# Optimization experiments

Measured on AMD Instinct MI355X. Metric: run time of the kernel, lower is better.

## Reference

```python
import jax, jax.numpy as jnp
import numpy as np

NEG = -1e30  # log(0) surrogate, safe for fp32 logaddexp
BLANK = 0


def setup_inputs() -> dict:
    key = jax.random.key(0)
    k1, k2, k3 = jax.random.split(key, 3)
    T, B, C, S = 1024, 128, 256, 64
    logits = jax.random.normal(k1, (T, B, C), dtype=jnp.float32)
    log_probs = jax.nn.log_softmax(logits, axis=-1)  # CTCLoss expects log-probs
    targets = jax.random.randint(k2, (B, S), 1, C)          # labels in [1, C-1], blank excluded
    target_lengths = jax.random.randint(k3, (B,), 1, S + 1)  # lengths in [1, S]
    return {"log_probs": log_probs, "targets": targets, "target_lengths": target_lengths}


def _ctc_loss(log_probs, targets, target_lengths):
    """CTC loss, blank=0, reduction='mean' (per-sample loss / target_len, then batch mean),
    zero_infinity=True, input_lengths = T for every batch element (as in the wrapper)."""
    T, B, C = log_probs.shape
    S = targets.shape[1]
    L = 2 * S + 1  # extended label length (blanks interleaved)

    # Extended label sequence: [blank, t0, blank, t1, ..., t_{S-1}, blank]  -> (B, L)
    ext = jnp.full((B, L), BLANK, dtype=targets.dtype)
    ext = ext.at[:, 1::2].set(targets)

    # Skip transition (s-2 -> s) allowed iff ext[s] != blank and ext[s] != ext[s-2]
    ext_m2 = jnp.concatenate([jnp.full((B, 2), BLANK, dtype=ext.dtype), ext[:, :-2]], axis=1)
    skip = (ext != BLANK) & (ext != ext_m2)
    skip = skip.at[:, :2].set(False)

    # alpha init at t=0
    lp0 = jnp.take_along_axis(log_probs[0], ext, axis=1)  # (B, L)
    alpha0 = jnp.full((B, L), NEG, dtype=log_probs.dtype)
    alpha0 = alpha0.at[:, 0].set(lp0[:, 0]).at[:, 1].set(lp0[:, 1])

    neg_col = jnp.full((B, 1), NEG, dtype=log_probs.dtype)

    def step(alpha, lp_t):
        lp_ext = jnp.take_along_axis(lp_t, ext, axis=1)            # (B, L)
        p1 = jnp.concatenate([neg_col, alpha[:, :-1]], axis=1)     # alpha[s-1]
        p2 = jnp.concatenate([neg_col, neg_col, alpha[:, :-2]], axis=1)  # alpha[s-2]
        a = jnp.logaddexp(alpha, p1)
        a = jnp.where(skip, jnp.logaddexp(a, p2), a)
        return a + lp_ext, None

    alpha, _ = jax.lax.scan(step, alpha0, log_probs[1:])  # (B, L)

    # Terminal states: s = 2*len and s = 2*len - 1
    idx_last = (2 * target_lengths)[:, None]
    a_last = jnp.take_along_axis(alpha, idx_last, axis=1)[:, 0]
    a_prev = jnp.take_along_axis(alpha, idx_last - 1, axis=1)[:, 0]
    loss = -jnp.logaddexp(a_last, a_prev)  # (B,)

    # zero_infinity=True: infinite (or NEG-saturated) losses -> 0
    loss = jnp.where(jnp.isfinite(loss) & (loss < 1e29), loss, 0.0)

    # reduction='mean': divide each loss by its target length, then mean over batch
    return jnp.mean(loss / target_lengths.astype(loss.dtype))


def reference(log_probs, targets, target_lengths):
    return _ctc_loss(log_probs, targets, target_lengths)
```

## Files before the change

kernel.cpp:

```cpp
#include <hip/hip_runtime.h>
#include <math.h>

#define LOG2E  1.4426950408889634f
#define LN2    0.6931471805599453f

#define T_DIM 1024
#define B_DIM 128
#define C_DIM 256
#define S_DIM 64
#define CH 16
#define NCHD 32
#define RBN 3
#define PBN 3

__device__ __forceinline__ float fexp2(float x) { return __builtin_amdgcn_exp2f(x); }
__device__ __forceinline__ float flog2(float x) { return __builtin_amdgcn_logf(x); }

__device__ __forceinline__ int dpp_shr1_i(int x) {
    return __builtin_amdgcn_update_dpp(0, x, 0x138, 0xF, 0xF, false);
}
__device__ __forceinline__ int dpp_shl1_i(int x) {
    return __builtin_amdgcn_update_dpp(0, x, 0x130, 0xF, 0xF, false);
}
template <int C> __device__ __forceinline__ float dpp_maxf(float m) {
    int s = __builtin_amdgcn_update_dpp(__float_as_int(m), __float_as_int(m),
                                        C, 0xF, 0xF, false);
    return fmaxf(m, __int_as_float(s));
}
template <int C> __device__ __forceinline__ float dpp_addf(float v) {
    int s = __builtin_amdgcn_update_dpp(0, __float_as_int(v), C, 0xF, 0xF, false);
    return v + __int_as_float(s);
}

#define GLOAD_LDS16(gp, lp)                                                    \
    __builtin_amdgcn_global_load_lds(                                          \
        (const __attribute__((address_space(1))) void*)(gp),                   \
        (__attribute__((address_space(3))) void*)(lp), 16, 0, 0)

#define VMWAIT(N_) asm volatile("s_waitcnt vmcnt(" #N_ ")" ::: "memory")
#define LGKM0()    asm volatile("s_waitcnt lgkmcnt(0)" ::: "memory")
#define FENCE()                                                                \
    do { __builtin_amdgcn_sched_barrier(0);                                    \
         asm volatile("" ::: "memory"); } while (0)

__global__ __launch_bounds__(512) void ctc_alpha_kernel(
    const float* __restrict__ log_probs,
    const int* __restrict__ targets,
    const int* __restrict__ target_lengths,
    float* __restrict__ per_batch)
{
    const int b = blockIdx.x;
    const int tid = threadIdx.x;
    const int lane = tid & 63;
    const int wid = tid >> 6;

    __shared__ float  rbF[RBN][CH][C_DIM];
    __shared__ float  rbB[RBN][CH][C_DIM];
    __shared__ float2 pcF[PBN][CH][64];
    __shared__ float2 pcB[PBN][CH][64];
    __shared__ float gam0[64], gam1[64];
    __shared__ int   gelB[64];
    __shared__ float gam2s;
    __shared__ int sfF, cvEF, cvOF, cfF, sfB, cvEB, cvOB, cfB;

    const int e1 = targets[b * S_DIM + lane];
    const int ep = (lane > 0) ? targets[b * S_DIM + lane - 1] : 0;
    const bool skipf = (lane > 0) && (e1 != ep);
    const int en = dpp_shl1_i(e1);
    const bool skipb = (lane < 63) && (en != e1);
    const bool is63 = (lane == 63);
    const int len = target_lengths[b];

    const float* base = log_probs + (size_t)b * C_DIM;
    const size_t stride = (size_t)B_DIM * C_DIM;

    if (tid == 0) {
        sfF = 0; cvEF = 0; cvOF = 0; cfF = 0;
        sfB = 0; cvEB = 0; cvOB = 0; cfB = 0;
    }
    __syncthreads();

    volatile int* vsfF = &sfF; volatile int* vcEF = &cvEF;
    volatile int* vcOF = &cvOF; volatile int* vcfF = &cfF;
    volatile int* vsfB = &sfB; volatile int* vcEB = &cvEB;
    volatile int* vcOB = &cvOB; volatile int* vcfB = &cfB;

#define STAGER_BODY(RB_, VSF_, VCE_, VCO_, T0_, SGN_)                          \
    do {                                                                       \
        for (int c = 0; c < NCHD; ++c) {                                       \
            if (c >= RBN) {                                                    \
                const int d_ = c - RBN;                                        \
                if (d_ & 1) { while (*VCO_ < (d_ + 1) / 2) __builtin_amdgcn_s_sleep(1); } \
                else        { while (*VCE_ < d_ / 2 + 1) __builtin_amdgcn_s_sleep(1); }  \
                FENCE();                                                       \
            }                                                                  \
            const int rb_ = c % RBN;                                           \
            _Pragma("unroll")                                                  \
            for (int k_ = 0; k_ < CH; ++k_) {                                  \
                const int t_ = (T0_) + (SGN_) * (16 * c + k_);                 \
                GLOAD_LDS16(base + (size_t)t_ * stride + 4 * lane,             \
                            &RB_[rb_][k_][0]);                                 \
            }                                                                  \
            VMWAIT(32);                                                        \
            FENCE();                                                           \
            if (c >= 2 && lane == 0) *VSF_ = c - 1;                            \
        }                                                                      \
        VMWAIT(16); FENCE(); if (lane == 0) *VSF_ = NCHD - 1;                  \
        VMWAIT(0);  FENCE(); if (lane == 0) *VSF_ = NCHD;                      \
    } while (0)

#define CONV_BODY(RB_, PC_, VSF_, VMYF_, VCF_, PAR_)                           \
    do {                                                                       \
        for (int c = PAR_; c < NCHD; c += 2) {                                 \
            while (*VSF_ < c + 1) { }                                          \
            if (c >= PBN) {                                                    \
                while (*VCF_ < c - PBN + 1) __builtin_amdgcn_s_sleep(1);       \
            }                                                                  \
            FENCE();                                                           \
            const int rb_ = c % RBN;                                           \
            const int pb_ = c % PBN;                                           \
            _Pragma("unroll")                                                  \
            for (int k_ = 0; k_ < CH; ++k_) {                                  \
                float pl_ = RB_[rb_][k_][e1];                                  \
                float pbl_ = RB_[rb_][k_][0];                                  \
                float2 v_;                                                     \
                v_.x = fexp2(pl_ * LOG2E);                                     \
                v_.y = fexp2(pbl_ * LOG2E);                                    \
                PC_[pb_][k_][lane] = v_;                                       \
            }                                                                  \
            LGKM0();                                                           \
            if (lane == 0) *VMYF_ = (PAR_) ? (c + 1) / 2 : c / 2 + 1;          \
        }                                                                      \
    } while (0)

#define POLLG(VCE_, VCO_, C_)                                                  \
    do { const int cc_ = (C_);                                                 \
         if (cc_ & 1) { while (*VCO_ < (cc_ + 1) / 2) { } }                    \
         else         { while (*VCE_ < cc_ / 2 + 1) { } }                      \
         FENCE(); } while (0)

#define GATHER_G(PC_, PLX, PBX, SLOT)                                          \
    do { _Pragma("unroll")                                                     \
         for (int k_ = 0; k_ < CH; ++k_) {                                     \
             float2 v_ = PC_[SLOT][k_][lane];                                  \
             PLX[k_] = v_.x; PBX[k_] = v_.y;                                   \
         } } while (0)

    if (wid == 1) {
        STAGER_BODY(rbF, vsfF, vcEF, vcOF, 1, 1);
    } else if (wid == 5) {
        STAGER_BODY(rbB, vsfB, vcEB, vcOB, 1022, -1);
    } else if (wid == 2) {
        CONV_BODY(rbF, pcF, vsfF, vcEF, vcfF, 0);
    } else if (wid == 3) {
        CONV_BODY(rbF, pcF, vsfF, vcOF, vcfF, 1);
    } else if (wid == 6) {
        CONV_BODY(rbB, pcB, vsfB, vcEB, vcfB, 0);
    } else if (wid == 7) {
        CONV_BODY(rbB, pcB, vsfB, vcOB, vcfB, 1);
    } else if (wid == 0) {
        float a0, a1, a2; int el = 0, dexp = 0;
        {
            float i0 = base[0], ie = base[e1];
            a0 = (lane == 0) ? fexp2(i0 * LOG2E) : 0.0f;
            a1 = (lane == 0) ? fexp2(ie * LOG2E) : 0.0f;
            a2 = 0.0f;
        }
#define RESCALE_F()                                                            \
    do { float mx_ = fmaxf(a0, fmaxf(a1, a2));                                 \
         int eb_ = (int)((__float_as_uint(mx_) >> 23) & 0xFFu) - 127;          \
         el += eb_;                                                            \
         float sc_ = __uint_as_float((unsigned)(127 - eb_) << 23);             \
         a0 *= sc_; a1 *= sc_; a2 *= sc_; } while (0)
#define ACT_STEP_F(PBV, PLV, K_)                                               \
    do { float am1_ = __int_as_float(dpp_shr1_i(__float_as_int(a1)));          \
         int eprev_ = dpp_shr1_i(el);                                          \
         int iz_ = __float_as_int(a0) | __float_as_int(a1) |                   \
                   __float_as_int(a2);                                         \
         int ele_ = (iz_ == 0) ? eprev_ : el;                                  \
         float am1s_ = ldexpf(am1_, eprev_ - ele_);                            \
         el = ele_;                                                            \
         float n0_ = (a0 + am1s_) * (PBV);                                     \
         float s2_ = skipf ? am1s_ : 0.0f;                                     \
         float n1_ = (a1 + a0 + s2_) * (PLV);                                  \
         float n2_ = (a2 + a1) * (PBV);                                        \
         a0 = n0_; a1 = n1_; a2 = n2_;                                         \
         if (((K_) & 3) == 3) RESCALE_F(); } while (0)
#define STREAM_STEP_F(PBV, PLV)                                                \
    do { float am1_ = __int_as_float(dpp_shr1_i(__float_as_int(a1)));          \
         float am1s_ = ldexpf(am1_, dexp);                                     \
         float n0_ = (a0 + am1s_) * (PBV);                                     \
         float s2_ = skipf ? am1s_ : 0.0f;                                     \
         float n1_ = (a1 + a0 + s2_) * (PLV);                                  \
         float n2_ = (a2 + a1) * (PBV);                                        \
         a0 = n0_; a1 = n1_; a2 = n2_; } while (0)
#define ACT_FROM_F(PLX, PBX)                                                   \
    do { _Pragma("unroll")                                                     \
         for (int k_ = 0; k_ < CH; ++k_) ACT_STEP_F(PBX[k_], PLX[k_], k_);     \
    } while (0)
#define STREAM_FROM_F(PLX, PBX)                                                \
    do { _Pragma("unroll")                                                     \
         for (int q_ = 0; q_ < 4; ++q_) {                                      \
             dexp = dpp_shr1_i(el) - el;                                       \
             STREAM_STEP_F(PBX[4 * q_ + 0], PLX[4 * q_ + 0]);                  \
             STREAM_STEP_F(PBX[4 * q_ + 1], PLX[4 * q_ + 1]);                  \
             STREAM_STEP_F(PBX[4 * q_ + 2], PLX[4 * q_ + 2]);                  \
             STREAM_STEP_F(PBX[4 * q_ + 3], PLX[4 * q_ + 3]);                  \
             RESCALE_F(); } } while (0)
#define TAIL_FROM_F(PLX, PBX)                                                  \
    do { _Pragma("unroll")                                                     \
         for (int q_ = 0; q_ < 3; ++q_) {                                      \
             dexp = dpp_shr1_i(el) - el;                                       \
             STREAM_STEP_F(PBX[4 * q_ + 0], PLX[4 * q_ + 0]);                  \
             STREAM_STEP_F(PBX[4 * q_ + 1], PLX[4 * q_ + 1]);                  \
             STREAM_STEP_F(PBX[4 * q_ + 2], PLX[4 * q_ + 2]);                  \
             STREAM_STEP_F(PBX[4 * q_ + 3], PLX[4 * q_ + 3]);                  \
             RESCALE_F(); }                                                    \
         dexp = dpp_shr1_i(el) - el;                                           \
         STREAM_STEP_F(PBX[12], PLX[12]);                                      \
         STREAM_STEP_F(PBX[13], PLX[13]);                                      \
         STREAM_STEP_F(PBX[14], PLX[14]); } while (0)

        float plA[CH], pbA[CH], plB[CH], pbB[CH];
        POLLG(vcEF, vcOF, 0);
        GATHER_G(pcF, plA, pbA, 0);
        for (int c = 0; c < 10; c += 2) {
            POLLG(vcEF, vcOF, c + 1);
            GATHER_G(pcF, plB, pbB, (c + 1) % PBN);
            ACT_FROM_F(plA, pbA);
            if (lane == 0) *vcfF = c + 1;
            POLLG(vcEF, vcOF, c + 2);
            GATHER_G(pcF, plA, pbA, (c + 2) % PBN);
            ACT_FROM_F(plB, pbB);
            if (lane == 0) *vcfF = c + 2;
        }
        for (int c = 10; c < 30; c += 2) {
            POLLG(vcEF, vcOF, c + 1);
            GATHER_G(pcF, plB, pbB, (c + 1) % PBN);
            STREAM_FROM_F(plA, pbA);
            if (lane == 0) *vcfF = c + 1;
            POLLG(vcEF, vcOF, c + 2);
            GATHER_G(pcF, plA, pbA, (c + 2) % PBN);
            STREAM_FROM_F(plB, pbB);
            if (lane == 0) *vcfF = c + 2;
        }
        POLLG(vcEF, vcOF, NCHD - 1);
        GATHER_G(pcF, plB, pbB, (NCHD - 1) % PBN);
        STREAM_FROM_F(plA, pbA);
        if (lane == 0) *vcfF = NCHD - 1;
        TAIL_FROM_F(plB, pbB);
        if (lane == 0) *vcfF = NCHD;

        __syncthreads();

        float la0 = flog2(a0) + (float)el;
        float la1 = flog2(a1) + (float)el;
        float g0 = gam0[lane], g1 = gam1[lane];
        float eB = (float)gelB[lane];
        float q0 = la0 + flog2(g0) + eB;
        float q1 = la1 + flog2(g1) + eB;
        float q2 = is63 ? (flog2(a2) + (float)el + flog2(gam2s) + eB) : -1e30f;
        q0 = fmaxf(q0, -1e30f); q1 = fmaxf(q1, -1e30f); q2 = fmaxf(q2, -1e30f);
        float ml = fmaxf(q0, fmaxf(q1, q2));
        float lw = ml + flog2(fexp2(q0 - ml) + fexp2(q1 - ml) + fexp2(q2 - ml));
        float m_ = lw;
        m_ = dpp_maxf<0x111>(m_); m_ = dpp_maxf<0x112>(m_);
        m_ = dpp_maxf<0x114>(m_); m_ = dpp_maxf<0x118>(m_);
        m_ = dpp_maxf<0x142>(m_); m_ = dpp_maxf<0x143>(m_);
        float M = __int_as_float(__builtin_amdgcn_readlane(__float_as_int(m_), 63));
        float v_ = fexp2(lw - M);
        v_ = dpp_addf<0x111>(v_); v_ = dpp_addf<0x112>(v_);
        v_ = dpp_addf<0x114>(v_); v_ = dpp_addf<0x118>(v_);
        v_ = dpp_addf<0x142>(v_); v_ = dpp_addf<0x143>(v_);
        float S = __int_as_float(__builtin_amdgcn_readlane(__float_as_int(v_), 63));
        if (lane == 0) {
            float lse2 = M + flog2(S);
            float loss = -(lse2 * LN2);
            if (!isfinite(loss) || !(loss < 1e29f)) loss = 0.0f;
            per_batch[b] = loss / (float)len;
        }
    } else {
        float b0, b1, b2; int elB = 0, dexB = 0, dex0 = 0;
        {
            const float* rowT = base + (size_t)(T_DIM - 1) * stride;
            float lpb_ = rowT[0], lpl_ = rowT[e1];
            b1 = (lane == len - 1) ? fexp2(lpl_ * LOG2E) : 0.0f;
            b0 = (lane == len && len < S_DIM) ? fexp2(lpb_ * LOG2E) : 0.0f;
            b2 = (len == S_DIM && is63) ? fexp2(lpb_ * LOG2E) : 0.0f;
        }
#define RESCALE_B()                                                            \
    do { float mx_ = fmaxf(b0, fmaxf(b1, b2));                                 \
         int eb_ = (int)((__float_as_uint(mx_) >> 23) & 0xFFu) - 127;          \
         elB += eb_;                                                           \
         float sc_ = __uint_as_float((unsigned)(127 - eb_) << 23);             \
         b0 *= sc_; b1 *= sc_; b2 *= sc_; } while (0)
#define ACT_STEP_B(PBV, PLV, K_)                                               \
    do { float nb0_ = __int_as_float(dpp_shl1_i(__float_as_int(b0)));          \
         nb0_ = is63 ? b2 : nb0_;                                              \
         float nb1_ = __int_as_float(dpp_shl1_i(__float_as_int(b1)));          \
         int en_ = dpp_shl1_i(elB);                                            \
         int iz_ = __float_as_int(b0) | __float_as_int(b1) |                   \
                   __float_as_int(b2);                                         \
         int eln_ = (iz_ == 0) ? en_ : elB;                                    \
         int d0_ = is63 ? (elB - eln_) : (en_ - eln_);                         \
         float nb0a_ = ldexpf(nb0_, d0_);                                      \
         float nb1a_ = ldexpf(nb1_, en_ - eln_);                               \
         elB = eln_;                                                           \
         float n0_ = (b0 + b1) * (PBV);                                        \
         float n1_ = (b1 + nb0a_ + (skipb ? nb1a_ : 0.0f)) * (PLV);            \
         float n2_ = b2 * (PBV);                                               \
         b0 = n0_; b1 = n1_; b2 = n2_;                                         \
         if (((K_) & 3) == 3) RESCALE_B(); } while (0)
#define STREAM_STEP_B(PBV, PLV)                                                \
    do { float nb0_ = __int_as_float(dpp_shl1_i(__float_as_int(b0)));          \
         nb0_ = is63 ? b2 : nb0_;                                              \
         float nb1_ = __int_as_float(dpp_shl1_i(__float_as_int(b1)));          \
         float nb0a_ = ldexpf(nb0_, dex0);                                     \
         float nb1a_ = ldexpf(nb1_, dexB);                                     \
         float n0_ = (b0 + b1) * (PBV);                                        \
         float n1_ = (b1 + nb0a_ + (skipb ? nb1a_ : 0.0f)) * (PLV);            \
         float n2_ = b2 * (PBV);                                               \
         b0 = n0_; b1 = n1_; b2 = n2_; } while (0)
#define SET_DEX_B()                                                            \
    do { dexB = dpp_shl1_i(elB) - elB; dex0 = is63 ? 0 : dexB; } while (0)
#define ACT_FROM_B(PLX, PBX)                                                   \
    do { _Pragma("unroll")                                                     \
         for (int k_ = 0; k_ < CH; ++k_) ACT_STEP_B(PBX[k_], PLX[k_], k_);     \
    } while (0)
#define STREAM_FROM_B(PLX, PBX)                                                \
    do { _Pragma("unroll")                                                     \
         for (int q_ = 0; q_ < 4; ++q_) {                                      \
             SET_DEX_B();                                                      \
             STREAM_STEP_B(PBX[4 * q_ + 0], PLX[4 * q_ + 0]);                  \
             STREAM_STEP_B(PBX[4 * q_ + 1], PLX[4 * q_ + 1]);                  \
             STREAM_STEP_B(PBX[4 * q_ + 2], PLX[4 * q_ + 2]);                  \
             STREAM_STEP_B(PBX[4 * q_ + 3], PLX[4 * q_ + 3]);                  \
             RESCALE_B(); } } while (0)
#define TAIL_FROM_B(PLX, PBX)                                                  \
    do { _Pragma("unroll")                                                     \
         for (int q_ = 0; q_ < 3; ++q_) {                                      \
             SET_DEX_B();                                                      \
             STREAM_STEP_B(PBX[4 * q_ + 0], PLX[4 * q_ + 0]);                  \
             STREAM_STEP_B(PBX[4 * q_ + 1], PLX[4 * q_ + 1]);                  \
             STREAM_STEP_B(PBX[4 * q_ + 2], PLX[4 * q_ + 2]);                  \
             STREAM_STEP_B(PBX[4 * q_ + 3], PLX[4 * q_ + 3]);                  \
             RESCALE_B(); }                                                    \
         SET_DEX_B();                                                          \
         STREAM_STEP_B(PBX[12], PLX[12]);                                      \
         STREAM_STEP_B(PBX[13], PLX[13]);                                      \
         STREAM_STEP_B(PBX[14], PLX[14]); } while (0)

        float plA[CH], pbA[CH], plB[CH], pbB[CH];
        POLLG(vcEB, vcOB, 0);
        GATHER_G(pcB, plA, pbA, 0);
        for (int c = 0; c < 10; c += 2) {
            POLLG(vcEB, vcOB, c + 1);
            GATHER_G(pcB, plB, pbB, (c + 1) % PBN);
            ACT_FROM_B(plA, pbA);
            if (lane == 0) *vcfB = c + 1;
            POLLG(vcEB, vcOB, c + 2);
            GATHER_G(pcB, plA, pbA, (c + 2) % PBN);
            ACT_FROM_B(plB, pbB);
            if (lane == 0) *vcfB = c + 2;
        }
        for (int c = 10; c < 30; c += 2) {
            POLLG(vcEB, vcOB, c + 1);
            GATHER_G(pcB, plB, pbB, (c + 1) % PBN);
            STREAM_FROM_B(plA, pbA);
            if (lane == 0) *vcfB = c + 1;
            POLLG(vcEB, vcOB, c + 2);
            GATHER_G(pcB, plA, pbA, (c + 2) % PBN);
            STREAM_FROM_B(plB, pbB);
            if (lane == 0) *vcfB = c + 2;
        }
        POLLG(vcEB, vcOB, NCHD - 1);
        GATHER_G(pcB, plB, pbB, (NCHD - 1) % PBN);
        STREAM_FROM_B(plA, pbA);
        if (lane == 0) *vcfB = NCHD - 1;
        TAIL_FROM_B(plB, pbB);
        if (lane == 0) *vcfB = NCHD;

        {
            float nb0_ = __int_as_float(dpp_shl1_i(__float_as_int(b0)));
            nb0_ = is63 ? b2 : nb0_;
            float nb1_ = __int_as_float(dpp_shl1_i(__float_as_int(b1)));
            int en_ = dpp_shl1_i(elB);
            int d_ = is63 ? 0 : (en_ - elB);
            float nb0a_ = ldexpf(nb0_, d_);
            float nb1a_ = ldexpf(nb1_, d_);
            gam0[lane] = b0 + b1;
            gam1[lane] = b1 + nb0a_ + (skipb ? nb1a_ : 0.0f);
            gelB[lane] = elB;
            if (is63) gam2s = b2;
        }
        __syncthreads();
    }

    if (wid != 0 && wid != 4) __syncthreads();
}

__global__ __launch_bounds__(64) void ctc_reduce_kernel(
    const float* __restrict__ per_batch, float* __restrict__ out)
{
    const int lane = threadIdx.x;
    float v = per_batch[lane] + per_batch[lane + 64];
    #pragma unroll
    for (int off = 32; off > 0; off >>= 1) {
        v += __shfl_down(v, off, 64);
    }
    if (lane == 0) out[0] = v / (float)B_DIM;
}

extern "C" void kernel_launch(void* const* d_in, const int* in_sizes, int n_in,
                              void* d_out, int out_size, void* d_ws, size_t ws_size,
                              hipStream_t stream) {
    const float* log_probs = (const float*)d_in[0];
    const int* targets = (const int*)d_in[1];
    const int* target_lengths = (const int*)d_in[2];
    float* out = (float*)d_out;
    float* per_batch = (float*)d_ws;

    ctc_alpha_kernel<<<B_DIM, 512, 0, stream>>>(log_probs, targets,
                                                target_lengths, per_batch);
    ctc_reduce_kernel<<<1, 64, 0, stream>>>(per_batch, out);
}
```

Baseline: 45.38 us.

## Split forward and backward CTC scans into separate workgroups, combine in second kernel

The single 512-thread block that ran both the forward alpha and backward beta recursions for one batch element is split into two 256-thread blocks, one per direction, giving 256 workgroups instead of 128. Each block writes log-domain boundary values to workspace, and a new combine kernel does the per-sample logsumexp, zero_infinity handling and batch mean, replacing the in-block meet and reduce. LDS ring depths are raised (RBN 4, PBN 6) because each block now holds only one direction's buffers. This aims to spread the serial scans across more CUs, at the cost of a global-memory round trip and a heavier final kernel that serially loops over 16 samples per wave.

```diff
diff --git a/kernel.cpp b/kernel.cpp
--- a/kernel.cpp
+++ b/kernel.cpp
@@ -10,8 +10,8 @@
 #define S_DIM 64
 #define CH 16
 #define NCHD 32
-#define RBN 3
-#define PBN 3
+#define RBN 4
+#define PBN 6
 
 __device__ __forceinline__ float fexp2(float x) { return __builtin_amdgcn_exp2f(x); }
 __device__ __forceinline__ float flog2(float x) { return __builtin_amdgcn_logf(x); }
@@ -21,15 +21,6 @@
 }
 __device__ __forceinline__ int dpp_shl1_i(int x) {
     return __builtin_amdgcn_update_dpp(0, x, 0x130, 0xF, 0xF, false);
-}
-template <int C> __device__ __forceinline__ float dpp_maxf(float m) {
-    int s = __builtin_amdgcn_update_dpp(__float_as_int(m), __float_as_int(m),
-                                        C, 0xF, 0xF, false);
-    return fmaxf(m, __int_as_float(s));
-}
-template <int C> __device__ __forceinline__ float dpp_addf(float v) {
-    int s = __builtin_amdgcn_update_dpp(0, __float_as_int(v), C, 0xF, 0xF, false);
-    return v + __int_as_float(s);
 }
 
 #define GLOAD_LDS16(gp, lp)                                                    \
@@ -43,25 +34,22 @@
     do { __builtin_amdgcn_sched_barrier(0);                                    \
          asm volatile("" ::: "memory"); } while (0)
 
-__global__ __launch_bounds__(512) void ctc_alpha_kernel(
+__global__ __launch_bounds__(256) void ctc_scan_kernel(
     const float* __restrict__ log_probs,
     const int* __restrict__ targets,
     const int* __restrict__ target_lengths,
-    float* __restrict__ per_batch)
+    float* __restrict__ ws)
 {
-    const int b = blockIdx.x;
+    const int bx = blockIdx.x;
+    const int b = bx >> 1;
+    const int dir = bx & 1;
     const int tid = threadIdx.x;
     const int lane = tid & 63;
     const int wid = tid >> 6;
 
-    __shared__ float  rbF[RBN][CH][C_DIM];
-    __shared__ float  rbB[RBN][CH][C_DIM];
-    __shared__ float2 pcF[PBN][CH][64];
-    __shared__ float2 pcB[PBN][CH][64];
-    __shared__ float gam0[64], gam1[64];
-    __shared__ int   gelB[64];
-    __shared__ float gam2s;
-    __shared__ int sfF, cvEF, cvOF, cfF, sfB, cvEB, cvOB, cfB;
+    __shared__ float  rbuf[RBN][CH][C_DIM];
+    __shared__ float2 pcv[PBN][CH][64];
+    __shared__ int sf, cvE, cvO, cf;
 
     const int e1 = targets[b * S_DIM + lane];
     const int ep = (lane > 0) ? targets[b * S_DIM + lane - 1] : 0;
@@ -74,91 +62,72 @@
     const float* base = log_probs + (size_t)b * C_DIM;
     const size_t stride = (size_t)B_DIM * C_DIM;
 
-    if (tid == 0) {
-        sfF = 0; cvEF = 0; cvOF = 0; cfF = 0;
-        sfB = 0; cvEB = 0; cvOB = 0; cfB = 0;
-    }
+    if (tid == 0) { sf = 0; cvE = 0; cvO = 0; cf = 0; }
     __syncthreads();
 
-    volatile int* vsfF = &sfF; volatile int* vcEF = &cvEF;
-    volatile int* vcOF = &cvOF; volatile int* vcfF = &cfF;
-    volatile int* vsfB = &sfB; volatile int* vcEB = &cvEB;
-    volatile int* vcOB = &cvOB; volatile int* vcfB = &cfB;
-
-#define STAGER_BODY(RB_, VSF_, VCE_, VCO_, T0_, SGN_)                          \
-    do {                                                                       \
-        for (int c = 0; c < NCHD; ++c) {                                       \
-            if (c >= RBN) {                                                    \
-                const int d_ = c - RBN;                                        \
-                if (d_ & 1) { while (*VCO_ < (d_ + 1) / 2) __builtin_amdgcn_s_sleep(1); } \
-                else        { while (*VCE_ < d_ / 2 + 1) __builtin_amdgcn_s_sleep(1); }  \
-                FENCE();                                                       \
-            }                                                                  \
-            const int rb_ = c % RBN;                                           \
-            _Pragma("unroll")                                                  \
-            for (int k_ = 0; k_ < CH; ++k_) {                                  \
-                const int t_ = (T0_) + (SGN_) * (16 * c + k_);                 \
-                GLOAD_LDS16(base + (size_t)t_ * stride + 4 * lane,             \
-                            &RB_[rb_][k_][0]);                                 \
-            }                                                                  \
-            VMWAIT(32);                                                        \
-            FENCE();                                                           \
-            if (c >= 2 && lane == 0) *VSF_ = c - 1;                            \
-        }                                                                      \
-        VMWAIT(16); FENCE(); if (lane == 0) *VSF_ = NCHD - 1;                  \
-        VMWAIT(0);  FENCE(); if (lane == 0) *VSF_ = NCHD;                      \
-    } while (0)
-
-#define CONV_BODY(RB_, PC_, VSF_, VMYF_, VCF_, PAR_)                           \
-    do {                                                                       \
-        for (int c = PAR_; c < NCHD; c += 2) {                                 \
-            while (*VSF_ < c + 1) { }                                          \
-            if (c >= PBN) {                                                    \
-                while (*VCF_ < c - PBN + 1) __builtin_amdgcn_s_sleep(1);       \
-            }                                                                  \
-            FENCE();                                                           \
-            const int rb_ = c % RBN;                                           \
-            const int pb_ = c % PBN;                                           \
-            _Pragma("unroll")                                                  \
-            for (int k_ = 0; k_ < CH; ++k_) {                                  \
-                float pl_ = RB_[rb_][k_][e1];                                  \
-                float pbl_ = RB_[rb_][k_][0];                                  \
-                float2 v_;                                                     \
-                v_.x = fexp2(pl_ * LOG2E);                                     \
-                v_.y = fexp2(pbl_ * LOG2E);                                    \
-                PC_[pb_][k_][lane] = v_;                                       \
-            }                                                                  \
-            LGKM0();                                                           \
-            if (lane == 0) *VMYF_ = (PAR_) ? (c + 1) / 2 : c / 2 + 1;          \
-        }                                                                      \
-    } while (0)
-
-#define POLLG(VCE_, VCO_, C_)                                                  \
+    volatile int* vsf = &sf; volatile int* vcE = &cvE;
+    volatile int* vcO = &cvO; volatile int* vcf = &cf;
+
+    const int t0d = dir ? 1022 : 1;
+    const int sgn = dir ? -1 : 1;
+
+#define POLLG(C_)                                                              \
     do { const int cc_ = (C_);                                                 \
-         if (cc_ & 1) { while (*VCO_ < (cc_ + 1) / 2) { } }                    \
-         else         { while (*VCE_ < cc_ / 2 + 1) { } }                      \
+         if (cc_ & 1) { while (*vcO < (cc_ + 1) / 2) { } }                     \
+         else         { while (*vcE < cc_ / 2 + 1) { } }                       \
          FENCE(); } while (0)
 
-#define GATHER_G(PC_, PLX, PBX, SLOT)                                          \
+#define GATHER_G(PLX, PBX, SLOT)                                               \
     do { _Pragma("unroll")                                                     \
          for (int k_ = 0; k_ < CH; ++k_) {                                     \
-             float2 v_ = PC_[SLOT][k_][lane];                                  \
+             float2 v_ = pcv[SLOT][k_][lane];                                  \
              PLX[k_] = v_.x; PBX[k_] = v_.y;                                   \
          } } while (0)
 
     if (wid == 1) {
-        STAGER_BODY(rbF, vsfF, vcEF, vcOF, 1, 1);
-    } else if (wid == 5) {
-        STAGER_BODY(rbB, vsfB, vcEB, vcOB, 1022, -1);
-    } else if (wid == 2) {
-        CONV_BODY(rbF, pcF, vsfF, vcEF, vcfF, 0);
-    } else if (wid == 3) {
-        CONV_BODY(rbF, pcF, vsfF, vcOF, vcfF, 1);
-    } else if (wid == 6) {
-        CONV_BODY(rbB, pcB, vsfB, vcEB, vcfB, 0);
-    } else if (wid == 7) {
-        CONV_BODY(rbB, pcB, vsfB, vcOB, vcfB, 1);
-    } else if (wid == 0) {
+        for (int c = 0; c < NCHD; ++c) {
+            if (c >= RBN) {
+                const int d_ = c - RBN;
+                if (d_ & 1) { while (*vcO < (d_ + 1) / 2) __builtin_amdgcn_s_sleep(1); }
+                else        { while (*vcE < d_ / 2 + 1) __builtin_amdgcn_s_sleep(1); }
+                FENCE();
+            }
+            const int rb_ = c & (RBN - 1);
+            #pragma unroll
+            for (int k_ = 0; k_ < CH; ++k_) {
+                const int t_ = t0d + sgn * (16 * c + k_);
+                GLOAD_LDS16(base + (size_t)t_ * stride + 4 * lane,
+                            &rbuf[rb_][k_][0]);
+            }
+            VMWAIT(32);
+            FENCE();
+            if (c >= 2 && lane == 0) *vsf = c - 1;
+        }
+        VMWAIT(16); FENCE(); if (lane == 0) *vsf = NCHD - 1;
+        VMWAIT(0);  FENCE(); if (lane == 0) *vsf = NCHD;
+    } else if (wid >= 2) {
+        const int par = wid - 2;
+        for (int c = par; c < NCHD; c += 2) {
+            while (*vsf < c + 1) { }
+            if (c >= PBN) {
+                while (*vcf < c - PBN + 1) __builtin_amdgcn_s_sleep(1);
+            }
+            FENCE();
+            const int rb_ = c & (RBN - 1);
+            const int pb_ = c % PBN;
+            #pragma unroll
+            for (int k_ = 0; k_ < CH; ++k_) {
+                float pl_ = rbuf[rb_][k_][e1];
+                float pbl_ = rbuf[rb_][k_][0];
+                float2 v_;
+                v_.x = fexp2(pl_ * LOG2E);
+                v_.y = fexp2(pbl_ * LOG2E);
+                pcv[pb_][k_][lane] = v_;
+            }
+            LGKM0();
+            if (lane == 0) { if (par) *vcO = (c + 1) / 2; else *vcE = c / 2 + 1; }
+        }
+    } else if (dir == 0) {
         float a0, a1, a2; int el = 0, dexp = 0;
         {
             float i0 = base[0], ie = base[e1];
@@ -222,63 +191,31 @@
          STREAM_STEP_F(PBX[14], PLX[14]); } while (0)
 
         float plA[CH], pbA[CH], plB[CH], pbB[CH];
-        POLLG(vcEF, vcOF, 0);
-        GATHER_G(pcF, plA, pbA, 0);
+        POLLG(0);
+        GATHER_G(plA, pbA, 0);
         for (int c = 0; c < 10; c += 2) {
-            POLLG(vcEF, vcOF, c + 1);
-            GATHER_G(pcF, plB, pbB, (c + 1) % PBN);
-            ACT_FROM_F(plA, pbA);
-            if (lane == 0) *vcfF = c + 1;
-            POLLG(vcEF, vcOF, c + 2);
-            GATHER_G(pcF, plA, pbA, (c + 2) % PBN);
-            ACT_FROM_F(plB, pbB);
-            if (lane == 0) *vcfF = c + 2;
+            POLLG(c + 1); GATHER_G(plB, pbB, (c + 1) % PBN);
+            ACT_FROM_F(plA, pbA); if (lane == 0) *vcf = c + 1;
+            POLLG(c + 2); GATHER_G(plA, pbA, (c + 2) % PBN);
+            ACT_FROM_F(plB, pbB); if (lane == 0) *vcf = c + 2;
         }
         for (int c = 10; c < 30; c += 2) {
-            POLLG(vcEF, vcOF, c + 1);
-            GATHER_G(pcF, plB, pbB, (c + 1) % PBN);
-            STREAM_FROM_F(plA, pbA);
-            if (lane == 0) *vcfF = c + 1;
-            POLLG(vcEF, vcOF, c + 2);
-            GATHER_G(pcF, plA, pbA, (c + 2) % PBN);
-            STREAM_FROM_F(plB, pbB);
-            if (lane == 0) *vcfF = c + 2;
-        }
-        POLLG(vcEF, vcOF, NCHD - 1);
-        GATHER_G(pcF, plB, pbB, (NCHD - 1) % PBN);
+            POLLG(c + 1); GATHER_G(plB, pbB, (c + 1) % PBN);
+            STREAM_FROM_F(plA, pbA); if (lane == 0) *vcf = c + 1;
+            POLLG(c + 2); GATHER_G(plA, pbA, (c + 2) % PBN);
+            STREAM_FROM_F(plB, pbB); if (lane == 0) *vcf = c + 2;
+        }
+        POLLG(NCHD - 1);
+        GATHER_G(plB, pbB, (NCHD - 1) % PBN);
         STREAM_FROM_F(plA, pbA);
-        if (lane == 0) *vcfF = NCHD - 1;
+        if (lane == 0) *vcf = NCHD - 1;
         TAIL_FROM_F(plB, pbB);
-        if (lane == 0) *vcfF = NCHD;
-
-        __syncthreads();
-
-        float la0 = flog2(a0) + (float)el;
-        float la1 = flog2(a1) + (float)el;
-        float g0 = gam0[lane], g1 = gam1[lane];
-        float eB = (float)gelB[lane];
-        float q0 = la0 + flog2(g0) + eB;
-        float q1 = la1 + flog2(g1) + eB;
-        float q2 = is63 ? (flog2(a2) + (float)el + flog2(gam2s) + eB) : -1e30f;
-        q0 = fmaxf(q0, -1e30f); q1 = fmaxf(q1, -1e30f); q2 = fmaxf(q2, -1e30f);
-        float ml = fmaxf(q0, fmaxf(q1, q2));
-        float lw = ml + flog2(fexp2(q0 - ml) + fexp2(q1 - ml) + fexp2(q2 - ml));
-        float m_ = lw;
-        m_ = dpp_maxf<0x111>(m_); m_ = dpp_maxf<0x112>(m_);
-        m_ = dpp_maxf<0x114>(m_); m_ = dpp_maxf<0x118>(m_);
-        m_ = dpp_maxf<0x142>(m_); m_ = dpp_maxf<0x143>(m_);
-        float M = __int_as_float(__builtin_amdgcn_readlane(__float_as_int(m_), 63));
-        float v_ = fexp2(lw - M);
-        v_ = dpp_addf<0x111>(v_); v_ = dpp_addf<0x112>(v_);
-        v_ = dpp_addf<0x114>(v_); v_ = dpp_addf<0x118>(v_);
-        v_ = dpp_addf<0x142>(v_); v_ = dpp_addf<0x143>(v_);
-        float S = __int_as_float(__builtin_amdgcn_readlane(__float_as_int(v_), 63));
-        if (lane == 0) {
-            float lse2 = M + flog2(S);
-            float loss = -(lse2 * LN2);
-            if (!isfinite(loss) || !(loss < 1e29f)) loss = 0.0f;
-            per_batch[b] = loss / (float)len;
-        }
+        if (lane == 0) *vcf = NCHD;
+
+        float* oF = ws + (size_t)b * 129;
+        oF[lane] = flog2(a0) + (float)el;
+        oF[64 + lane] = flog2(a1) + (float)el;
+        if (is63) oF[128] = flog2(a2) + (float)el;
     } else {
         float b0, b1, b2; int elB = 0, dexB = 0, dex0 = 0;
         {
@@ -351,34 +288,26 @@
          STREAM_STEP_B(PBX[14], PLX[14]); } while (0)
 
         float plA[CH], pbA[CH], plB[CH], pbB[CH];
-        POLLG(vcEB, vcOB, 0);
-        GATHER_G(pcB, plA, pbA, 0);
+        POLLG(0);
+        GATHER_G(plA, pbA, 0);
         for (int c = 0; c < 10; c += 2) {
-            POLLG(vcEB, vcOB, c + 1);
-            GATHER_G(pcB, plB, pbB, (c + 1) % PBN);
-            ACT_FROM_B(plA, pbA);
-            if (lane == 0) *vcfB = c + 1;
-            POLLG(vcEB, vcOB, c + 2);
-            GATHER_G(pcB, plA, pbA, (c + 2) % PBN);
-            ACT_FROM_B(plB, pbB);
-            if (lane == 0) *vcfB = c + 2;
+            POLLG(c + 1); GATHER_G(plB, pbB, (c + 1) % PBN);
+            ACT_FROM_B(plA, pbA); if (lane == 0) *vcf = c + 1;
+            POLLG(c + 2); GATHER_G(plA, pbA, (c + 2) % PBN);
+            ACT_FROM_B(plB, pbB); if (lane == 0) *vcf = c + 2;
         }
         for (int c = 10; c < 30; c += 2) {
-            POLLG(vcEB, vcOB, c + 1);
-            GATHER_G(pcB, plB, pbB, (c + 1) % PBN);
-            STREAM_FROM_B(plA, pbA);
-            if (lane == 0) *vcfB = c + 1;
-            POLLG(vcEB, vcOB, c + 2);
-            GATHER_G(pcB, plA, pbA, (c + 2) % PBN);
-            STREAM_FROM_B(plB, pbB);
-            if (lane == 0) *vcfB = c + 2;
-        }
-        POLLG(vcEB, vcOB, NCHD - 1);
-        GATHER_G(pcB, plB, pbB, (NCHD - 1) % PBN);
+            POLLG(c + 1); GATHER_G(plB, pbB, (c + 1) % PBN);
+            STREAM_FROM_B(plA, pbA); if (lane == 0) *vcf = c + 1;
+            POLLG(c + 2); GATHER_G(plA, pbA, (c + 2) % PBN);
+            STREAM_FROM_B(plB, pbB); if (lane == 0) *vcf = c + 2;
+        }
+        POLLG(NCHD - 1);
+        GATHER_G(plB, pbB, (NCHD - 1) % PBN);
         STREAM_FROM_B(plA, pbA);
-        if (lane == 0) *vcfB = NCHD - 1;
+        if (lane == 0) *vcf = NCHD - 1;
         TAIL_FROM_B(plB, pbB);
-        if (lane == 0) *vcfB = NCHD;
+        if (lane == 0) *vcf = NCHD;
 
         {
             float nb0_ = __int_as_float(dpp_shl1_i(__float_as_int(b0)));
@@ -388,27 +317,57 @@
             int d_ = is63 ? 0 : (en_ - elB);
             float nb0a_ = ldexpf(nb0_, d_);
             float nb1a_ = ldexpf(nb1_, d_);
-            gam0[lane] = b0 + b1;
-            gam1[lane] = b1 + nb0a_ + (skipb ? nb1a_ : 0.0f);
-            gelB[lane] = elB;
-            if (is63) gam2s = b2;
-        }
-        __syncthreads();
+            float g0 = b0 + b1;
+            float g1 = b1 + nb0a_ + (skipb ? nb1a_ : 0.0f);
+            float* oB = ws + (size_t)(B_DIM * 129) + (size_t)b * 129;
+            oB[lane] = flog2(g0) + (float)elB;
+            oB[64 + lane] = flog2(g1) + (float)elB;
+            if (is63) oB[128] = flog2(b2) + (float)elB;
+        }
     }
-
-    if (wid != 0 && wid != 4) __syncthreads();
-}
-
-__global__ __launch_bounds__(64) void ctc_reduce_kernel(
-    const float* __restrict__ per_batch, float* __restrict__ out)
+}
+
+__global__ __launch_bounds__(512) void ctc_combine_kernel(
+    const float* __restrict__ ws,
+    const int* __restrict__ target_lengths,
+    float* __restrict__ out)
 {
-    const int lane = threadIdx.x;
-    float v = per_batch[lane] + per_batch[lane + 64];
-    #pragma unroll
-    for (int off = 32; off > 0; off >>= 1) {
-        v += __shfl_down(v, off, 64);
+    const int tid = threadIdx.x;
+    const int lane = tid & 63;
+    const int w = tid >> 6;
+    __shared__ float part[8];
+
+    float acc = 0.0f;
+    for (int i = 0; i < 16; ++i) {
+        const int b = w * 16 + i;
+        const float* F = ws + (size_t)b * 129;
+        const float* G = ws + (size_t)(B_DIM * 129) + (size_t)b * 129;
+        float q0 = F[lane] + G[lane];
+        float q1 = F[64 + lane] + G[64 + lane];
+        float q2 = (lane == 63) ? (F[128] + G[128]) : -1e30f;
+        float m = fmaxf(q0, fmaxf(q1, q2));
+        #pragma unroll
+        for (int off = 1; off < 64; off <<= 1) {
+            m = fmaxf(m, __shfl_xor(m, off, 64));
+        }
+        float s = fexp2(q0 - m) + fexp2(q1 - m) + fexp2(q2 - m);
+        #pragma unroll
+        for (int off = 1; off < 64; off <<= 1) {
+            s += __shfl_xor(s, off, 64);
+        }
+        float lse2 = m + flog2(s);
+        float loss = -(lse2 * LN2);
+        if (!isfinite(loss) || !(loss < 1e29f)) loss = 0.0f;
+        acc += loss / (float)target_lengths[b];
     }
-    if (lane == 0) out[0] = v / (float)B_DIM;
+    if (lane == 0) part[w] = acc;
+    __syncthreads();
+    if (tid == 0) {
+        float t = 0.0f;
+        #pragma unroll
+        for (int i = 0; i < 8; ++i) t += part[i];
+        out[0] = t / (float)B_DIM;
+    }
 }
 
 extern "C" void kernel_launch(void* const* d_in, const int* in_sizes, int n_in,
@@ -418,9 +377,9 @@
     const int* targets = (const int*)d_in[1];
     const int* target_lengths = (const int*)d_in[2];
     float* out = (float*)d_out;
-    float* per_batch = (float*)d_ws;
-
-    ctc_alpha_kernel<<<B_DIM, 512, 0, stream>>>(log_probs, targets,
-                                                target_lengths, per_batch);
-    ctc_reduce_kernel<<<1, 64, 0, stream>>>(per_batch, out);
-}
+    float* ws = (float*)d_ws;
+
+    ctc_scan_kernel<<<2 * B_DIM, 256, 0, stream>>>(log_probs, targets,
+                                                   target_lengths, ws);
+    ctc_combine_kernel<<<1, 512, 0, stream>>>(ws, target_lengths, out);
+}
```

Measured after the change: 48.59 us. +7.1%, slower.
